# Performance work log

Hardware: AMD Instinct MI355X
Metric: run time of the kernel (lower is better)

## Reference

```python
import jax, jax.numpy as jnp
import numpy as np

N_NODES = 100000

def gcn_conv(x, edge_index, W, b):
    # torch_geometric GCNConv: add self-loops, sym-normalize, aggregate, add bias
    n = x.shape[0]
    loop = jnp.arange(n)
    src = jnp.concatenate([edge_index[0], loop])  # [E+N]
    dst = jnp.concatenate([edge_index[1], loop])
    h = x @ W  # [N, out]
    deg = jax.ops.segment_sum(jnp.ones_like(dst, dtype=h.dtype), dst, num_segments=n)
    dinv = jnp.where(deg > 0, jax.lax.rsqrt(deg), 0.0)
    norm = dinv[src] * dinv[dst]  # [E+N]
    msg = h[src] * norm[:, None]  # gather + scale
    out = jax.ops.segment_sum(msg, dst, num_segments=n)  # scatter-add
    return out + b

def setup_inputs() -> dict:
    key = jax.random.key(0)
    ks = jax.random.split(key, 6)
    N, F, H, C, E = N_NODES, 128, 128, 32, 1600000
    x = jax.random.normal(ks[0], (N, F), dtype=jnp.float32)
    edge_index = jax.random.randint(ks[1], (2, E), 0, N, dtype=jnp.int64)
    W1 = jax.random.normal(ks[2], (F, H), dtype=jnp.float32) * (1.0 / np.sqrt(F))
    b1 = jnp.zeros((H,), jnp.float32)
    W2 = jax.random.normal(ks[3], (H, H), dtype=jnp.float32) * (1.0 / np.sqrt(H))
    b2 = jnp.zeros((H,), jnp.float32)
    Wc = jax.random.normal(ks[4], (H, C), dtype=jnp.float32) * (1.0 / np.sqrt(H))
    bc = jnp.zeros((C,), jnp.float32)
    return {"x": x, "edge_index": edge_index, "W1": W1, "b1": b1, "W2": W2, "b2": b2, "Wc": Wc, "bc": bc}

def reference(x, edge_index, W1, b1, W2, b2, Wc, bc):
    h = jax.nn.relu(gcn_conv(x, edge_index, W1, b1))
    # dropout is identity in eval mode
    h = jax.nn.relu(gcn_conv(h, edge_index, W2, b2))
    pooled = jnp.mean(h, axis=0)  # [H]
    return pooled @ Wc + bc  # [C]
```

## Files before the change

### kernel.cpp

```cpp
#include <hip/hip_runtime.h>
#include <hip/hip_bf16.h>


#define FEAT 128
#define CHUNK 4096
#define MAXBUCK 512
#define ECAP 12288
#define PBLK 512
#define BPAD 16384

typedef __attribute__((ext_vector_type(8))) short short8;
typedef __attribute__((ext_vector_type(4))) float float4v;
typedef __attribute__((ext_vector_type(2))) float floatx2;

union I4S8 { int4 i; short8 s; };

static __device__ inline unsigned short f2bf(float f) {
    union { __hip_bfloat16 h; unsigned short u; } cv;
    cv.h = __float2bfloat16(f);
    return cv.u;
}

static __device__ inline floatx2 fp8x2_dec(unsigned int u) {
#if __has_builtin(__builtin_amdgcn_cvt_pk_f32_fp8)
    return __builtin_amdgcn_cvt_pk_f32_fp8((int)u, false);
#else
    floatx2 r;
    unsigned int b0 = u & 0xFFu, b1 = (u >> 8) & 0xFFu;
    r.x = __uint_as_float(((b0 & 0x80u) << 24) | ((b0 & 0x7Fu) << 20)) * 0x1p+120f;
    r.y = __uint_as_float(((b1 & 0x80u) << 24) | ((b1 & 0x7Fu) << 20)) * 0x1p+120f;
    return r;
#endif
}

static __device__ inline floatx2 fp8x2_dec_hi(unsigned int u) {
#if __has_builtin(__builtin_amdgcn_cvt_pk_f32_fp8)
    return __builtin_amdgcn_cvt_pk_f32_fp8((int)u, true);
#else
    return fp8x2_dec(u >> 16);
#endif
}

static __device__ inline unsigned short fp8x2_enc(float x, float y) {
#if __has_builtin(__builtin_amdgcn_cvt_pk_fp8_f32)
    return (unsigned short)(__builtin_amdgcn_cvt_pk_fp8_f32(x, y, 0, false) & 0xFFFF);
#else
    auto enc1 = [](float f) -> unsigned int {
        unsigned int u = __float_as_uint(f);
        unsigned int s = (u >> 24) & 0x80u;
        float a = fabsf(f);
        a = fminf(a, 448.0f);
        unsigned int code;
        if (a < 0.015625f) {
            code = (unsigned int)(int)rintf(a * 512.0f);
        } else {
            unsigned int au = __float_as_uint(a);
            unsigned int r = au + 0x0007FFFFu + ((au >> 20) & 1u);
            unsigned int e = (r >> 23) - 120u;
            unsigned int m = (r >> 20) & 7u;
            code = (e << 3) | m;
            if (code > 0x7Eu) code = 0x7Eu;
        }
        return code | s;
    };
    return (unsigned short)(enc1(x) | (enc1(y) << 8));
#endif
}

static __device__ inline unsigned char fp8enc(float f) {
#if __has_builtin(__builtin_amdgcn_cvt_pk_fp8_f32)
    return (unsigned char)(__builtin_amdgcn_cvt_pk_fp8_f32(f, 0.0f, 0, false) & 0xFF);
#else
    return (unsigned char)(fp8x2_enc(f, 0.0f) & 0xFF);
#endif
}

__global__ __launch_bounds__(256) void hist2(const int* __restrict__ dst,
                                             int* __restrict__ hist,
                                             int nE, int NC, int nbuck) {
    __shared__ int h[MAXBUCK];
    int c = blockIdx.x, t = threadIdx.x;
    for (int i = t; i < nbuck; i += 256) h[i] = 0;
    __syncthreads();
    int beg = c * CHUNK, end = min(nE, beg + CHUNK);
    for (int e = beg + t; e < end; e += 256)
        atomicAdd(&h[dst[e] >> 8], 1);
    __syncthreads();
    for (int i = t; i < nbuck; i += 256) hist[i * NC + c] = h[i];
}

__global__ __launch_bounds__(256) void rowsum_k(const int* __restrict__ hist,
                                                int* __restrict__ btot, int NC) {
    __shared__ int red[256];
    int b = blockIdx.x, t = threadIdx.x;
    int s = 0;
    for (int c = t; c < NC; c += 256) s += hist[b * NC + c];
    red[t] = s;
    __syncthreads();
    for (int o = 128; o > 0; o >>= 1) {
        if (t < o) red[t] += red[t + o];
        __syncthreads();
    }
    if (t == 0) btot[b] = red[0];
}

__global__ __launch_bounds__(512) void bscan_k(const int* __restrict__ btot,
                                               int* __restrict__ bboff, int nbuck) {
    __shared__ int sc[512];
    int t = threadIdx.x;
    int v = (t < nbuck) ? btot[t] : 0;
    sc[t] = v;
    __syncthreads();
    for (int o = 1; o < 512; o <<= 1) {
        int add = (t >= o) ? sc[t - o] : 0;
        __syncthreads();
        sc[t] += add;
        __syncthreads();
    }
    if (t < nbuck) {
        bboff[t] = sc[t] - v;
        if (t == nbuck - 1) bboff[nbuck] = sc[t];
    }
}

__global__ __launch_bounds__(512) void rowoff_k(const int* __restrict__ hist,
                                                const int* __restrict__ bboff,
                                                int* __restrict__ hoff, int NC) {
    __shared__ int sc[512];
    int b = blockIdx.x, t = threadIdx.x;
    int v = (t < NC) ? hist[b * NC + t] : 0;
    sc[t] = v;
    __syncthreads();
    for (int o = 1; o < 512; o <<= 1) {
        int add = (t >= o) ? sc[t - o] : 0;
        __syncthreads();
        sc[t] += add;
        __syncthreads();
    }
    if (t < NC) hoff[b * NC + t] = bboff[b] + sc[t] - v;
}

__global__ __launch_bounds__(256) void fill2(const int* __restrict__ src,
                                             const int* __restrict__ dst,
                                             const int* __restrict__ off,
                                             int* __restrict__ binned,
                                             int nE, int NC, int nbuck) {
    __shared__ int cur[MAXBUCK];
    int c = blockIdx.x, t = threadIdx.x;
    for (int i = t; i < nbuck; i += 256) cur[i] = off[i * NC + c];
    __syncthreads();
    int beg = c * CHUNK, end = min(nE, beg + CHUNK);
    for (int e = beg + t; e < end; e += 256) {
        int d = dst[e];
        int pos = atomicAdd(&cur[d >> 8], 1);
        binned[pos] = (src[e] << 8) | (d & 255);
    }
}

__global__ __launch_bounds__(256) void bucket_scat(const int* __restrict__ binned,
                                                   const int* __restrict__ bboff,
                                                   int* __restrict__ cnt,
                                                   float* __restrict__ dinv,
                                                   int* __restrict__ cursor,
                                                   int* __restrict__ csr_src, int n) {
    __shared__ int se[ECAP];
    __shared__ int lcnt[256];
    __shared__ int lcur[256];
    __shared__ int ssc[256];
    __shared__ int poff[128];
    int b = blockIdx.x, t = threadIdx.x;
    int node0 = b << 8;
    int nloc = min(256, n - node0);
    int ebeg = bboff[b], eend = bboff[b + 1];
    int ne = eend - ebeg;
    int pbase = (ebeg + b * BPAD + 15) & ~15;
    int zOff = n << 7;
    lcnt[t] = 0;
    lcur[t] = 0;
    __syncthreads();
    bool staged = (ne <= ECAP);
    if (staged) {
        for (int i = t; i < ne; i += 256) {
            int e = binned[ebeg + i];
            se[i] = e;
            atomicAdd(&lcnt[e & 255], 1);
        }
    } else {
        for (int i = t; i < ne; i += 256)
            atomicAdd(&lcnt[binned[ebeg + i] & 255], 1);
    }
    __syncthreads();
    int myc = (t < nloc) ? lcnt[t] : 0;
    int npair = (nloc + 1) >> 1;
    int pairSlots = 0;
    if (t < npair) {
        int mx = max(lcnt[2 * t], lcnt[2 * t + 1]);
        pairSlots = 2 * ((mx + 15) & ~15);
    }
    ssc[t] = pairSlots;
    __syncthreads();
    for (int o = 1; o < 256; o <<= 1) {
        int add = (t >= o) ? ssc[t - o] : 0;
        __syncthreads();
        ssc[t] += add;
        __syncthreads();
    }
    if (t < npair) poff[t] = ssc[t] - pairSlots;
    __syncthreads();
    if (t < nloc) {
        int p = t >> 1;
        int pl = ((max(lcnt[p * 2], lcnt[p * 2 + 1]) + 15) & ~15);
        cnt[node0 + t] = pl;
        dinv[node0 + t] = rsqrtf((float)(myc + 1));
        cursor[node0 + t] = pbase + poff[p];
    }
    __syncthreads();
    if (staged) {
        for (int i = t; i < ne; i += 256) {
            int e = se[i];
            int loc = e & 255;
            int q = atomicAdd(&lcur[loc], 1);
            int slot = pbase + poff[loc >> 1] + ((q >> 4) << 5) + ((loc & 1) << 4) + (q & 15);
            csr_src[slot] = (int)(((unsigned int)e >> 8) << 7);
        }
    } else {
        for (int i = t; i < ne; i += 256) {
            int e = binned[ebeg + i];
            int loc = e & 255;
            int q = atomicAdd(&lcur[loc], 1);
            int slot = pbase + poff[loc >> 1] + ((q >> 4) << 5) + ((loc & 1) << 4) + (q & 15);
            csr_src[slot] = (int)(((unsigned int)e >> 8) << 7);
        }
    }
    int nlocp = (nloc + 1) & ~1;
    if (t < nlocp) {
        int p = t >> 1, h = t & 1;
        int pl = ((max(lcnt[p * 2], lcnt[p * 2 + 1]) + 15) & ~15);
        int base = pbase + poff[p] + (h << 4);
        for (int q = myc; q < pl; q++)
            csr_src[base + ((q >> 4) << 5) + (q & 15)] = zOff;
    }
}

__global__ __launch_bounds__(256) void wprep2(const float* __restrict__ W1,
                                              const float* __restrict__ W2,
                                              unsigned short* __restrict__ Wbf1,
                                              unsigned short* __restrict__ Wbf2,
                                              unsigned char* __restrict__ gbuf,
                                              int n) {
    int tid = blockIdx.x * 256 + threadIdx.x;
    if (tid < 32)
        ((unsigned int*)(gbuf + (size_t)n * FEAT))[tid] = 0u;
    const float* W = (tid < 16384) ? W1 : W2;
    unsigned short* O = (tid < 16384) ? Wbf1 : Wbf2;
    int id = tid & 16383;
    int chunk = id >> 3, j = id & 7;
    int kb = chunk >> 7, nn = chunk & 127;
    O[id] = f2bf(W[(kb * 8 + j) * FEAT + nn]);
}

template <bool AFP32>
__global__ __launch_bounds__(256) void gemm_mfma(const void* __restrict__ Xv,
                                                 const unsigned short* __restrict__ Wbf,
                                                 const float* __restrict__ dinv,
                                                 unsigned char* __restrict__ gout,
                                                 int n) {
    int wave = threadIdx.x >> 6, lane = threadIdx.x & 63;
    int m0 = blockIdx.x * 64 + wave * 16;
    if (m0 >= n) return;
    int col = lane & 15, quad = lane >> 4;
    int mc = min(m0 + col, n - 1);

    short8 afr[4];
    if (AFP32) {
        const float* X = (const float*)Xv;
        const float* xr = X + (size_t)mc * FEAT + quad * 8;
#pragma unroll
        for (int ks = 0; ks < 4; ks++) {
            float4 lo = *(const float4*)(xr + ks * 32);
            float4 hi = *(const float4*)(xr + ks * 32 + 4);
            short8 a;
            a[0] = (short)f2bf(lo.x); a[1] = (short)f2bf(lo.y);
            a[2] = (short)f2bf(lo.z); a[3] = (short)f2bf(lo.w);
            a[4] = (short)f2bf(hi.x); a[5] = (short)f2bf(hi.y);
            a[6] = (short)f2bf(hi.z); a[7] = (short)f2bf(hi.w);
            afr[ks] = a;
        }
    } else {
        const unsigned char* X8 = (const unsigned char*)Xv;
        const unsigned char* xr = X8 + (size_t)mc * FEAT + quad * 8;
#pragma unroll
        for (int ks = 0; ks < 4; ks++) {
            uint2 u2 = *(const uint2*)(xr + ks * 32);
            floatx2 p0 = fp8x2_dec(u2.x);
            floatx2 p1 = fp8x2_dec_hi(u2.x);
            floatx2 p2 = fp8x2_dec(u2.y);
            floatx2 p3 = fp8x2_dec_hi(u2.y);
            short8 a;
            a[0] = (short)f2bf(p0.x); a[1] = (short)f2bf(p0.y);
            a[2] = (short)f2bf(p1.x); a[3] = (short)f2bf(p1.y);
            a[4] = (short)f2bf(p2.x); a[5] = (short)f2bf(p2.y);
            a[6] = (short)f2bf(p3.x); a[7] = (short)f2bf(p3.y);
            afr[ks] = a;
        }
    }

    float dvr[4];
#pragma unroll
    for (int r = 0; r < 4; r++)
        dvr[r] = dinv[min(m0 + quad * 4 + r, n - 1)];

    const int4* Wb = (const int4*)Wbf;
#pragma unroll
    for (int nt = 0; nt < 8; nt++) {
        float4v acc = {0.f, 0.f, 0.f, 0.f};
#pragma unroll
        for (int ks = 0; ks < 4; ks++) {
            int kb = ks * 4 + quad;
            I4S8 u; u.i = Wb[kb * FEAT + nt * 16 + col];
            acc = __builtin_amdgcn_mfma_f32_16x16x32_bf16(afr[ks], u.s, acc, 0, 0, 0);
        }
#pragma unroll
        for (int r = 0; r < 4; r++) {
            int row = m0 + quad * 4 + r;
            if (row < n)
                gout[(size_t)row * FEAT + nt * 16 + col] = fp8enc(acc[r] * dvr[r]);
        }
    }
}

__global__ __launch_bounds__(256) void agg_csr(const int* __restrict__ cursor,
                                               const int* __restrict__ cnt,
                                               const int* __restrict__ csr_src,
                                               const unsigned char* __restrict__ gbuf,
                                               const float* __restrict__ dinv,
                                               const float* __restrict__ bias,
                                               unsigned char* __restrict__ outb,
                                               int n) {
    int pair = blockIdx.x * 4 + (threadIdx.x >> 6);
    int nodeA = pair << 1;
    if (nodeA >= n) return;
    unsigned lane = threadIdx.x & 63;
    unsigned half = lane >> 5;
    unsigned sub = lane & 31;
    int node = nodeA + (int)half;
    unsigned fb = sub << 2;

    int curS = __builtin_amdgcn_readfirstlane(cursor[nodeA]);
    int plS = __builtin_amdgcn_readfirstlane(cnt[nodeA]);
    const unsigned char* csrB = (const unsigned char*)csr_src;
    const unsigned char* ip0 = csrB + (((size_t)(unsigned)curS) << 2) + (half << 6);

    unsigned su = *(const unsigned*)(gbuf + ((((unsigned)node) << 7) | fb));
    floatx2 a01 = fp8x2_dec(su), a23 = fp8x2_dec_hi(su);
    floatx2 b01 = {0.f, 0.f}, b23 = {0.f, 0.f};

    int rounds = plS >> 4;
    for (int r = 0; r < rounds; r++) {
        const unsigned char* p = ip0 + ((size_t)(unsigned)r << 7);
        int4 w0 = *(const int4*)(p);
        int4 w1 = *(const int4*)(p + 16);
        int4 w2 = *(const int4*)(p + 32);
        int4 w3 = *(const int4*)(p + 48);
        unsigned uu[16];
        uu[0]  = *(const unsigned*)(gbuf + ((unsigned)w0.x | fb));
        uu[1]  = *(const unsigned*)(gbuf + ((unsigned)w0.y | fb));
        uu[2]  = *(const unsigned*)(gbuf + ((unsigned)w0.z | fb));
        uu[3]  = *(const unsigned*)(gbuf + ((unsigned)w0.w | fb));
        uu[4]  = *(const unsigned*)(gbuf + ((unsigned)w1.x | fb));
        uu[5]  = *(const unsigned*)(gbuf + ((unsigned)w1.y | fb));
        uu[6]  = *(const unsigned*)(gbuf + ((unsigned)w1.z | fb));
        uu[7]  = *(const unsigned*)(gbuf + ((unsigned)w1.w | fb));
        uu[8]  = *(const unsigned*)(gbuf + ((unsigned)w2.x | fb));
        uu[9]  = *(const unsigned*)(gbuf + ((unsigned)w2.y | fb));
        uu[10] = *(const unsigned*)(gbuf + ((unsigned)w2.z | fb));
        uu[11] = *(const unsigned*)(gbuf + ((unsigned)w2.w | fb));
        uu[12] = *(const unsigned*)(gbuf + ((unsigned)w3.x | fb));
        uu[13] = *(const unsigned*)(gbuf + ((unsigned)w3.y | fb));
        uu[14] = *(const unsigned*)(gbuf + ((unsigned)w3.z | fb));
        uu[15] = *(const unsigned*)(gbuf + ((unsigned)w3.w | fb));
#pragma unroll
        for (int k = 0; k < 16; k += 2) {
            a01 += fp8x2_dec(uu[k]);
            a23 += fp8x2_dec_hi(uu[k]);
            b01 += fp8x2_dec(uu[k + 1]);
            b23 += fp8x2_dec_hi(uu[k + 1]);
        }
    }
    a01 += b01;
    a23 += b23;
    float dv = dinv[node];
    float4 bv = ((const float4*)bias)[sub];
    float r0 = fmaxf(a01.x * dv + bv.x, 0.0f);
    float r1 = fmaxf(a01.y * dv + bv.y, 0.0f);
    float r2 = fmaxf(a23.x * dv + bv.z, 0.0f);
    float r3 = fmaxf(a23.y * dv + bv.w, 0.0f);
    unsigned outw = (unsigned)fp8x2_enc(r0, r1) | ((unsigned)fp8x2_enc(r2, r3) << 16);
    *(unsigned*)(outb + ((((unsigned)node) << 7) | fb)) = outw;
}

__global__ __launch_bounds__(256) void pool_kernel(const unsigned char* __restrict__ a,
                                                   float* __restrict__ partial, int n) {
    __shared__ float red[16][132];
    int t = threadIdx.x, b = blockIdx.x;
    int fg = t & 15;
    int rg = t >> 4;
    unsigned fb = (unsigned)fg << 3;
    floatx2 s01 = {0.f, 0.f}, s23 = {0.f, 0.f}, s45 = {0.f, 0.f}, s67 = {0.f, 0.f};
    for (int i = (b << 4) | rg; i < n; i += PBLK * 16) {
        uint2 u2 = *(const uint2*)(a + (((unsigned)i << 7) | fb));
        s01 += fp8x2_dec(u2.x);
        s23 += fp8x2_dec_hi(u2.x);
        s45 += fp8x2_dec(u2.y);
        s67 += fp8x2_dec_hi(u2.y);
    }
    red[rg][fb + 0] = s01.x; red[rg][fb + 1] = s01.y;
    red[rg][fb + 2] = s23.x; red[rg][fb + 3] = s23.y;
    red[rg][fb + 4] = s45.x; red[rg][fb + 5] = s45.y;
    red[rg][fb + 6] = s67.x; red[rg][fb + 7] = s67.y;
    __syncthreads();
    if (t < FEAT) {
        float s = 0.0f;
#pragma unroll
        for (int k = 0; k < 16; k++) s += red[k][t];
        partial[b * FEAT + t] = s;
    }
}

__global__ __launch_bounds__(128) void final_kernel(const float* __restrict__ partial,
                                                    const float* __restrict__ Wc,
                                                    const float* __restrict__ bc,
                                                    float* __restrict__ out,
                                                    int n, int C) {
    __shared__ float p[FEAT];
    int t = threadIdx.x;
    float s = 0.0f;
    for (int b = 0; b < PBLK; b++) s += partial[b * FEAT + t];
    p[t] = s * (1.0f / (float)n);
    __syncthreads();
    if (t < C) {
        float acc = bc[t];
        for (int h = 0; h < FEAT; h++)
            acc += p[h] * Wc[h * C + t];
        out[t] = acc;
    }
}

extern "C" void kernel_launch(void* const* d_in, const int* in_sizes, int n_in,
                              void* d_out, int out_size, void* d_ws, size_t ws_size,
                              hipStream_t stream) {
    const float* x  = (const float*)d_in[0];
    const int*   ei = (const int*)d_in[1];
    const float* W1 = (const float*)d_in[2];
    const float* b1 = (const float*)d_in[3];
    const float* W2 = (const float*)d_in[4];
    const float* b2 = (const float*)d_in[5];
    const float* Wc = (const float*)d_in[6];
    const float* bc = (const float*)d_in[7];

    const int N = in_sizes[0] / FEAT;
    const int E = in_sizes[1] / 2;
    const int C = out_size;
    const int* srcI = ei;
    const int* dstI = ei + E;
    const int NC = (E + CHUNK - 1) / CHUNK;
    const int NBK = (N + 255) >> 8;
    const size_t csrCap = (size_t)E + (size_t)NBK * BPAD + 64;

    auto align256 = [](size_t v) { return (v + 255) & ~(size_t)255; };
    char* w = (char*)d_ws;
    int*            cnt     = (int*)w;            w += align256((size_t)N * 4);
    float*          dinv    = (float*)w;          w += align256((size_t)N * 4);
    int*            cursor  = (int*)w;            w += align256((size_t)N * 4);
    int*            csr_src = (int*)w;            w += align256(csrCap * 4);
    int*            binned  = (int*)w;            w += align256((size_t)E * 4);
    int*            hist    = (int*)w;            w += align256((size_t)NBK * NC * 4);
    int*            hoff    = (int*)w;            w += align256((size_t)NBK * NC * 4);
    int*            btot    = (int*)w;            w += align256((size_t)NBK * 4);
    int*            bboff   = (int*)w;            w += align256((size_t)(NBK + 1) * 4);
    unsigned short* Wbf1    = (unsigned short*)w; w += align256((size_t)FEAT * FEAT * 2);
    unsigned short* Wbf2    = (unsigned short*)w; w += align256((size_t)FEAT * FEAT * 2);
    unsigned char*  gbuf    = (unsigned char*)w;  w += align256((size_t)(N + 1) * FEAT);
    unsigned char*  bufA    = (unsigned char*)w;  w += align256((size_t)N * FEAT);
    float*          partial = (float*)w;          w += align256((size_t)PBLK * FEAT * 4);

    wprep2<<<128, 256, 0, stream>>>(W1, W2, Wbf1, Wbf2, gbuf, N);

    hist2<<<NC, 256, 0, stream>>>(dstI, hist, E, NC, NBK);
    rowsum_k<<<NBK, 256, 0, stream>>>(hist, btot, NC);
    bscan_k<<<1, 512, 0, stream>>>(btot, bboff, NBK);
    rowoff_k<<<NBK, 512, 0, stream>>>(hist, bboff, hoff, NC);
    fill2<<<NC, 256, 0, stream>>>(srcI, dstI, hoff, binned, E, NC, NBK);
    bucket_scat<<<NBK, 256, 0, stream>>>(binned, bboff, cnt, dinv, cursor, csr_src, N);

    const int gGemm = (N + 63) / 64;
    const int gAgg = (N + 7) / 8;

    gemm_mfma<true><<<gGemm, 256, 0, stream>>>(x, Wbf1, dinv, gbuf, N);
    agg_csr<<<gAgg, 256, 0, stream>>>(cursor, cnt, csr_src, gbuf, dinv, b1,
                                      bufA, N);

    gemm_mfma<false><<<gGemm, 256, 0, stream>>>(bufA, Wbf2, dinv, gbuf, N);
    agg_csr<<<gAgg, 256, 0, stream>>>(cursor, cnt, csr_src, gbuf, dinv, b2,
                                      bufA, N);

    pool_kernel<<<PBLK, 256, 0, stream>>>(bufA, partial, N);
    final_kernel<<<1, 128, 0, stream>>>(partial, Wc, bc, (float*)d_out, N, C);
}
```

Measured before the change: 266.6 us.

## Aggregate four nodes per wavefront with quad-interleaved padded CSR layout

The padded CSR layout now groups destination nodes in quads instead of pairs, interleaving 16-edge rounds for four nodes. Each wavefront aggregates four nodes, with 16 lanes per node each loading 8 fp8 features (uint2) instead of 4. This halves the number of wavefronts and makes each gather wider, but padding grows to the maximum degree among four nodes, adding dummy gathers, and the CSR buffer capacity is enlarged to match.

After: 283.2 us. 1.06x slower.

```diff
diff --git a/kernel.cpp b/kernel.cpp
--- a/kernel.cpp
+++ b/kernel.cpp
@@ -7,7 +7,7 @@
 #define MAXBUCK 512
 #define ECAP 12288
 #define PBLK 512
-#define BPAD 16384
+#define BPADQ 3904
 
 typedef __attribute__((ext_vector_type(8))) short short8;
 typedef __attribute__((ext_vector_type(4))) float float4v;
@@ -167,13 +167,13 @@
     __shared__ int lcnt[256];
     __shared__ int lcur[256];
     __shared__ int ssc[256];
-    __shared__ int poff[128];
+    __shared__ int qoff[64];
     int b = blockIdx.x, t = threadIdx.x;
     int node0 = b << 8;
     int nloc = min(256, n - node0);
     int ebeg = bboff[b], eend = bboff[b + 1];
     int ne = eend - ebeg;
-    int pbase = (ebeg + b * BPAD + 15) & ~15;
+    int pbase = (4 * ebeg + b * BPADQ + 15) & ~15;
     int zOff = n << 7;
     lcnt[t] = 0;
     lcur[t] = 0;
@@ -191,13 +191,14 @@
     }
     __syncthreads();
     int myc = (t < nloc) ? lcnt[t] : 0;
-    int npair = (nloc + 1) >> 1;
-    int pairSlots = 0;
-    if (t < npair) {
-        int mx = max(lcnt[2 * t], lcnt[2 * t + 1]);
-        pairSlots = 2 * ((mx + 15) & ~15);
-    }
-    ssc[t] = pairSlots;
+    int nquad = (nloc + 3) >> 2;
+    int quadSlots = 0;
+    if (t < nquad) {
+        int mx = max(max(lcnt[4 * t], lcnt[4 * t + 1]),
+                     max(lcnt[4 * t + 2], lcnt[4 * t + 3]));
+        quadSlots = ((mx + 15) & ~15) << 2;
+    }
+    ssc[t] = quadSlots;
     __syncthreads();
     for (int o = 1; o < 256; o <<= 1) {
         int add = (t >= o) ? ssc[t - o] : 0;
@@ -205,14 +206,15 @@
         ssc[t] += add;
         __syncthreads();
     }
-    if (t < npair) poff[t] = ssc[t] - pairSlots;
+    if (t < nquad) qoff[t] = ssc[t] - quadSlots;
     __syncthreads();
     if (t < nloc) {
-        int p = t >> 1;
-        int pl = ((max(lcnt[p * 2], lcnt[p * 2 + 1]) + 15) & ~15);
-        cnt[node0 + t] = pl;
+        int q = t >> 2;
+        int mx = max(max(lcnt[4 * q], lcnt[4 * q + 1]),
+                     max(lcnt[4 * q + 2], lcnt[4 * q + 3]));
+        cnt[node0 + t] = (mx + 15) & ~15;
         dinv[node0 + t] = rsqrtf((float)(myc + 1));
-        cursor[node0 + t] = pbase + poff[p];
+        cursor[node0 + t] = pbase + qoff[q];
     }
     __syncthreads();
     if (staged) {
@@ -220,7 +222,7 @@
             int e = se[i];
             int loc = e & 255;
             int q = atomicAdd(&lcur[loc], 1);
-            int slot = pbase + poff[loc >> 1] + ((q >> 4) << 5) + ((loc & 1) << 4) + (q & 15);
+            int slot = pbase + qoff[loc >> 2] + ((q >> 4) << 6) + ((loc & 3) << 4) + (q & 15);
             csr_src[slot] = (int)(((unsigned int)e >> 8) << 7);
         }
     } else {
@@ -228,17 +230,20 @@
             int e = binned[ebeg + i];
             int loc = e & 255;
             int q = atomicAdd(&lcur[loc], 1);
-            int slot = pbase + poff[loc >> 1] + ((q >> 4) << 5) + ((loc & 1) << 4) + (q & 15);
+            int slot = pbase + qoff[loc >> 2] + ((q >> 4) << 6) + ((loc & 3) << 4) + (q & 15);
             csr_src[slot] = (int)(((unsigned int)e >> 8) << 7);
         }
     }
-    int nlocp = (nloc + 1) & ~1;
-    if (t < nlocp) {
-        int p = t >> 1, h = t & 1;
-        int pl = ((max(lcnt[p * 2], lcnt[p * 2 + 1]) + 15) & ~15);
-        int base = pbase + poff[p] + (h << 4);
-        for (int q = myc; q < pl; q++)
-            csr_src[base + ((q >> 4) << 5) + (q & 15)] = zOff;
+    int nlocq = nquad << 2;
+    if (t < nlocq) {
+        int q = t >> 2, h = t & 3;
+        int mx = max(max(lcnt[4 * q], lcnt[4 * q + 1]),
+                     max(lcnt[4 * q + 2], lcnt[4 * q + 3]));
+        int ql = (mx + 15) & ~15;
+        int myc2 = (t < nloc) ? lcnt[t] : 0;
+        int base = pbase + qoff[q] + (h << 4);
+        for (int qp = myc2; qp < ql; qp++)
+            csr_src[base + ((qp >> 4) << 6) + (qp & 15)] = zOff;
     }
 }
 
@@ -337,66 +342,75 @@
                                                const float* __restrict__ bias,
                                                unsigned char* __restrict__ outb,
                                                int n) {
-    int pair = blockIdx.x * 4 + (threadIdx.x >> 6);
-    int nodeA = pair << 1;
+    int quad = blockIdx.x * 4 + (threadIdx.x >> 6);
+    int nodeA = quad << 2;
     if (nodeA >= n) return;
     unsigned lane = threadIdx.x & 63;
-    unsigned half = lane >> 5;
-    unsigned sub = lane & 31;
-    int node = nodeA + (int)half;
-    unsigned fb = sub << 2;
+    unsigned h = lane >> 4;
+    unsigned sub = lane & 15;
+    int node = nodeA + (int)h;
+    bool act = node < n;
+    int nodeC = act ? node : (n - 1);
+    unsigned fb = sub << 3;
 
     int curS = __builtin_amdgcn_readfirstlane(cursor[nodeA]);
-    int plS = __builtin_amdgcn_readfirstlane(cnt[nodeA]);
+    int qlS  = __builtin_amdgcn_readfirstlane(cnt[nodeA]);
     const unsigned char* csrB = (const unsigned char*)csr_src;
-    const unsigned char* ip0 = csrB + (((size_t)(unsigned)curS) << 2) + (half << 6);
-
-    unsigned su = *(const unsigned*)(gbuf + ((((unsigned)node) << 7) | fb));
-    floatx2 a01 = fp8x2_dec(su), a23 = fp8x2_dec_hi(su);
-    floatx2 b01 = {0.f, 0.f}, b23 = {0.f, 0.f};
-
-    int rounds = plS >> 4;
+    const unsigned char* ip0 = csrB + (((size_t)(unsigned)curS) << 2) + (h << 6);
+
+    uint2 su = *(const uint2*)(gbuf + ((((unsigned)nodeC) << 7) | fb));
+    floatx2 a01 = fp8x2_dec(su.x), a23 = fp8x2_dec_hi(su.x);
+    floatx2 a45 = fp8x2_dec(su.y), a67 = fp8x2_dec_hi(su.y);
+
+    int rounds = qlS >> 4;
     for (int r = 0; r < rounds; r++) {
-        const unsigned char* p = ip0 + ((size_t)(unsigned)r << 7);
+        const unsigned char* p = ip0 + ((size_t)(unsigned)r << 8);
         int4 w0 = *(const int4*)(p);
         int4 w1 = *(const int4*)(p + 16);
         int4 w2 = *(const int4*)(p + 32);
         int4 w3 = *(const int4*)(p + 48);
-        unsigned uu[16];
-        uu[0]  = *(const unsigned*)(gbuf + ((unsigned)w0.x | fb));
-        uu[1]  = *(const unsigned*)(gbuf + ((unsigned)w0.y | fb));
-        uu[2]  = *(const unsigned*)(gbuf + ((unsigned)w0.z | fb));
-        uu[3]  = *(const unsigned*)(gbuf + ((unsigned)w0.w | fb));
-        uu[4]  = *(const unsigned*)(gbuf + ((unsigned)w1.x | fb));
-        uu[5]  = *(const unsigned*)(gbuf + ((unsigned)w1.y | fb));
-        uu[6]  = *(const unsigned*)(gbuf + ((unsigned)w1.z | fb));
-        uu[7]  = *(const unsigned*)(gbuf + ((unsigned)w1.w | fb));
-        uu[8]  = *(const unsigned*)(gbuf + ((unsigned)w2.x | fb));
-        uu[9]  = *(const unsigned*)(gbuf + ((unsigned)w2.y | fb));
-        uu[10] = *(const unsigned*)(gbuf + ((unsigned)w2.z | fb));
-        uu[11] = *(const unsigned*)(gbuf + ((unsigned)w2.w | fb));
-        uu[12] = *(const unsigned*)(gbuf + ((unsigned)w3.x | fb));
-        uu[13] = *(const unsigned*)(gbuf + ((unsigned)w3.y | fb));
-        uu[14] = *(const unsigned*)(gbuf + ((unsigned)w3.z | fb));
-        uu[15] = *(const unsigned*)(gbuf + ((unsigned)w3.w | fb));
-#pragma unroll
-        for (int k = 0; k < 16; k += 2) {
-            a01 += fp8x2_dec(uu[k]);
-            a23 += fp8x2_dec_hi(uu[k]);
-            b01 += fp8x2_dec(uu[k + 1]);
-            b23 += fp8x2_dec_hi(uu[k + 1]);
-        }
-    }
-    a01 += b01;
-    a23 += b23;
-    float dv = dinv[node];
-    float4 bv = ((const float4*)bias)[sub];
-    float r0 = fmaxf(a01.x * dv + bv.x, 0.0f);
-    float r1 = fmaxf(a01.y * dv + bv.y, 0.0f);
-    float r2 = fmaxf(a23.x * dv + bv.z, 0.0f);
-    float r3 = fmaxf(a23.y * dv + bv.w, 0.0f);
-    unsigned outw = (unsigned)fp8x2_enc(r0, r1) | ((unsigned)fp8x2_enc(r2, r3) << 16);
-    *(unsigned*)(outb + ((((unsigned)node) << 7) | fb)) = outw;
+        uint2 uu[16];
+        uu[0]  = *(const uint2*)(gbuf + ((unsigned)w0.x | fb));
+        uu[1]  = *(const uint2*)(gbuf + ((unsigned)w0.y | fb));
+        uu[2]  = *(const uint2*)(gbuf + ((unsigned)w0.z | fb));
+        uu[3]  = *(const uint2*)(gbuf + ((unsigned)w0.w | fb));
+        uu[4]  = *(const uint2*)(gbuf + ((unsigned)w1.x | fb));
+        uu[5]  = *(const uint2*)(gbuf + ((unsigned)w1.y | fb));
+        uu[6]  = *(const uint2*)(gbuf + ((unsigned)w1.z | fb));
+        uu[7]  = *(const uint2*)(gbuf + ((unsigned)w1.w | fb));
+        uu[8]  = *(const uint2*)(gbuf + ((unsigned)w2.x | fb));
+        uu[9]  = *(const uint2*)(gbuf + ((unsigned)w2.y | fb));
+        uu[10] = *(const uint2*)(gbuf + ((unsigned)w2.z | fb));
+        uu[11] = *(const uint2*)(gbuf + ((unsigned)w2.w | fb));
+        uu[12] = *(const uint2*)(gbuf + ((unsigned)w3.x | fb));
+        uu[13] = *(const uint2*)(gbuf + ((unsigned)w3.y | fb));
+        uu[14] = *(const uint2*)(gbuf + ((unsigned)w3.z | fb));
+        uu[15] = *(const uint2*)(gbuf + ((unsigned)w3.w | fb));
+#pragma unroll
+        for (int k = 0; k < 16; k++) {
+            a01 += fp8x2_dec(uu[k].x);
+            a23 += fp8x2_dec_hi(uu[k].x);
+            a45 += fp8x2_dec(uu[k].y);
+            a67 += fp8x2_dec_hi(uu[k].y);
+        }
+    }
+    if (act) {
+        float dv = dinv[node];
+        const float4* b4 = (const float4*)bias;
+        float4 bv0 = b4[sub * 2], bv1 = b4[sub * 2 + 1];
+        float r0 = fmaxf(a01.x * dv + bv0.x, 0.0f);
+        float r1 = fmaxf(a01.y * dv + bv0.y, 0.0f);
+        float r2 = fmaxf(a23.x * dv + bv0.z, 0.0f);
+        float r3 = fmaxf(a23.y * dv + bv0.w, 0.0f);
+        float r4 = fmaxf(a45.x * dv + bv1.x, 0.0f);
+        float r5 = fmaxf(a45.y * dv + bv1.y, 0.0f);
+        float r6 = fmaxf(a67.x * dv + bv1.z, 0.0f);
+        float r7 = fmaxf(a67.y * dv + bv1.w, 0.0f);
+        uint2 ow;
+        ow.x = (unsigned)fp8x2_enc(r0, r1) | ((unsigned)fp8x2_enc(r2, r3) << 16);
+        ow.y = (unsigned)fp8x2_enc(r4, r5) | ((unsigned)fp8x2_enc(r6, r7) << 16);
+        *(uint2*)(outb + ((((unsigned)node) << 7) | fb)) = ow;
+    }
 }
 
 __global__ __launch_bounds__(256) void pool_kernel(const unsigned char* __restrict__ a,
@@ -465,7 +479,7 @@
     const int* dstI = ei + E;
     const int NC = (E + CHUNK - 1) / CHUNK;
     const int NBK = (N + 255) >> 8;
-    const size_t csrCap = (size_t)E + (size_t)NBK * BPAD + 64;
+    const size_t csrCap = (size_t)4 * E + (size_t)NBK * BPADQ + 64;
 
     auto align256 = [](size_t v) { return (v + 255) & ~(size_t)255; };
     char* w = (char*)d_ws;
@@ -494,7 +508,7 @@
     bucket_scat<<<NBK, 256, 0, stream>>>(binned, bboff, cnt, dinv, cursor, csr_src, N);
 
     const int gGemm = (N + 63) / 64;
-    const int gAgg = (N + 7) / 8;
+    const int gAgg = (N + 15) / 16;
 
     gemm_mfma<true><<<gGemm, 256, 0, stream>>>(x, Wbf1, dinv, gbuf, N);
     agg_csr<<<gAgg, 256, 0, stream>>>(cursor, cnt, csr_src, gbuf, dinv, b1,
```

## Replace bucketed two-pass CSR build with per-node global atomic histogram and scatter

Applied to the files above, without the earlier changes.

Replaces the chunked bucket histogram, row offsets, binning and per-bucket shared-memory scatter with a simpler pipeline. It counts in-degrees with global atomics per node, computes padded pair slots and bucket offsets from those counts, pads slots, then scatters edges directly with per-node global atomic cursors. This drops two kernels and the intermediate binned array, trading them for random global atomics and scattered writes into the CSR buffer.

Result: slower. 412.2 us (+54.6%).

```diff
diff --git a/kernel.cpp b/kernel.cpp
--- a/kernel.cpp
+++ b/kernel.cpp
@@ -3,11 +3,7 @@
 
 
 #define FEAT 128
-#define CHUNK 4096
-#define MAXBUCK 512
-#define ECAP 12288
 #define PBLK 512
-#define BPAD 16384
 
 typedef __attribute__((ext_vector_type(8))) short short8;
 typedef __attribute__((ext_vector_type(4))) float float4v;
@@ -75,33 +71,36 @@
 #endif
 }
 
-__global__ __launch_bounds__(256) void hist2(const int* __restrict__ dst,
-                                             int* __restrict__ hist,
-                                             int nE, int NC, int nbuck) {
-    __shared__ int h[MAXBUCK];
-    int c = blockIdx.x, t = threadIdx.x;
-    for (int i = t; i < nbuck; i += 256) h[i] = 0;
-    __syncthreads();
-    int beg = c * CHUNK, end = min(nE, beg + CHUNK);
-    for (int e = beg + t; e < end; e += 256)
-        atomicAdd(&h[dst[e] >> 8], 1);
-    __syncthreads();
-    for (int i = t; i < nbuck; i += 256) hist[i * NC + c] = h[i];
-}
-
-__global__ __launch_bounds__(256) void rowsum_k(const int* __restrict__ hist,
-                                                int* __restrict__ btot, int NC) {
-    __shared__ int red[256];
+__global__ __launch_bounds__(256) void histN(const int* __restrict__ dst,
+                                             int* __restrict__ cnt, int nE) {
+    int stride = gridDim.x * 256;
+    for (int e = blockIdx.x * 256 + threadIdx.x; e < nE; e += stride)
+        atomicAdd(&cnt[dst[e]], 1);
+}
+
+__global__ __launch_bounds__(256) void pairsum_k(const int* __restrict__ cnt,
+                                                 int* __restrict__ btot, int n) {
+    __shared__ int lcnt[256];
+    __shared__ int ssc[256];
     int b = blockIdx.x, t = threadIdx.x;
-    int s = 0;
-    for (int c = t; c < NC; c += 256) s += hist[b * NC + c];
-    red[t] = s;
-    __syncthreads();
-    for (int o = 128; o > 0; o >>= 1) {
-        if (t < o) red[t] += red[t + o];
-        __syncthreads();
-    }
-    if (t == 0) btot[b] = red[0];
+    int node0 = b << 8;
+    int nloc = min(256, n - node0);
+    lcnt[t] = (t < nloc) ? cnt[node0 + t] : 0;
+    __syncthreads();
+    int pairSlots = 0;
+    if (t < 128) {
+        int mx = max(lcnt[2 * t], lcnt[2 * t + 1]);
+        pairSlots = ((mx + 15) & ~15) << 1;
+    }
+    ssc[t] = pairSlots;
+    __syncthreads();
+    for (int o = 1; o < 256; o <<= 1) {
+        int add = (t >= o) ? ssc[t - o] : 0;
+        __syncthreads();
+        ssc[t] += add;
+        __syncthreads();
+    }
+    if (t == 255) btot[b] = ssc[255];
 }
 
 __global__ __launch_bounds__(512) void bscan_k(const int* __restrict__ btot,
@@ -123,79 +122,26 @@
     }
 }
 
-__global__ __launch_bounds__(512) void rowoff_k(const int* __restrict__ hist,
-                                                const int* __restrict__ bboff,
-                                                int* __restrict__ hoff, int NC) {
-    __shared__ int sc[512];
-    int b = blockIdx.x, t = threadIdx.x;
-    int v = (t < NC) ? hist[b * NC + t] : 0;
-    sc[t] = v;
-    __syncthreads();
-    for (int o = 1; o < 512; o <<= 1) {
-        int add = (t >= o) ? sc[t - o] : 0;
-        __syncthreads();
-        sc[t] += add;
-        __syncthreads();
-    }
-    if (t < NC) hoff[b * NC + t] = bboff[b] + sc[t] - v;
-}
-
-__global__ __launch_bounds__(256) void fill2(const int* __restrict__ src,
-                                             const int* __restrict__ dst,
-                                             const int* __restrict__ off,
-                                             int* __restrict__ binned,
-                                             int nE, int NC, int nbuck) {
-    __shared__ int cur[MAXBUCK];
-    int c = blockIdx.x, t = threadIdx.x;
-    for (int i = t; i < nbuck; i += 256) cur[i] = off[i * NC + c];
-    __syncthreads();
-    int beg = c * CHUNK, end = min(nE, beg + CHUNK);
-    for (int e = beg + t; e < end; e += 256) {
-        int d = dst[e];
-        int pos = atomicAdd(&cur[d >> 8], 1);
-        binned[pos] = (src[e] << 8) | (d & 255);
-    }
-}
-
-__global__ __launch_bounds__(256) void bucket_scat(const int* __restrict__ binned,
+__global__ __launch_bounds__(256) void cursorpad_k(int* __restrict__ cnt,
                                                    const int* __restrict__ bboff,
-                                                   int* __restrict__ cnt,
+                                                   int* __restrict__ cursor,
                                                    float* __restrict__ dinv,
-                                                   int* __restrict__ cursor,
+                                                   int* __restrict__ qcur,
                                                    int* __restrict__ csr_src, int n) {
-    __shared__ int se[ECAP];
     __shared__ int lcnt[256];
-    __shared__ int lcur[256];
     __shared__ int ssc[256];
     __shared__ int poff[128];
     int b = blockIdx.x, t = threadIdx.x;
     int node0 = b << 8;
     int nloc = min(256, n - node0);
-    int ebeg = bboff[b], eend = bboff[b + 1];
-    int ne = eend - ebeg;
-    int pbase = (ebeg + b * BPAD + 15) & ~15;
+    int pbase = bboff[b];
     int zOff = n << 7;
-    lcnt[t] = 0;
-    lcur[t] = 0;
-    __syncthreads();
-    bool staged = (ne <= ECAP);
-    if (staged) {
-        for (int i = t; i < ne; i += 256) {
-            int e = binned[ebeg + i];
-            se[i] = e;
-            atomicAdd(&lcnt[e & 255], 1);
-        }
-    } else {
-        for (int i = t; i < ne; i += 256)
-            atomicAdd(&lcnt[binned[ebeg + i] & 255], 1);
-    }
-    __syncthreads();
-    int myc = (t < nloc) ? lcnt[t] : 0;
-    int npair = (nloc + 1) >> 1;
+    lcnt[t] = (t < nloc) ? cnt[node0 + t] : 0;
+    __syncthreads();
     int pairSlots = 0;
-    if (t < npair) {
+    if (t < 128) {
         int mx = max(lcnt[2 * t], lcnt[2 * t + 1]);
-        pairSlots = 2 * ((mx + 15) & ~15);
+        pairSlots = ((mx + 15) & ~15) << 1;
     }
     ssc[t] = pairSlots;
     __syncthreads();
@@ -205,40 +151,38 @@
         ssc[t] += add;
         __syncthreads();
     }
-    if (t < npair) poff[t] = ssc[t] - pairSlots;
-    __syncthreads();
+    if (t < 128) poff[t] = ssc[t] - pairSlots;
+    __syncthreads();
+    int p = t >> 1, h = t & 1;
+    int pl = ((max(lcnt[p * 2], lcnt[p * 2 + 1]) + 15) & ~15);
     if (t < nloc) {
-        int p = t >> 1;
-        int pl = ((max(lcnt[p * 2], lcnt[p * 2 + 1]) + 15) & ~15);
+        int deg = lcnt[t];
         cnt[node0 + t] = pl;
-        dinv[node0 + t] = rsqrtf((float)(myc + 1));
+        dinv[node0 + t] = rsqrtf((float)(deg + 1));
         cursor[node0 + t] = pbase + poff[p];
-    }
-    __syncthreads();
-    if (staged) {
-        for (int i = t; i < ne; i += 256) {
-            int e = se[i];
-            int loc = e & 255;
-            int q = atomicAdd(&lcur[loc], 1);
-            int slot = pbase + poff[loc >> 1] + ((q >> 4) << 5) + ((loc & 1) << 4) + (q & 15);
-            csr_src[slot] = (int)(((unsigned int)e >> 8) << 7);
-        }
-    } else {
-        for (int i = t; i < ne; i += 256) {
-            int e = binned[ebeg + i];
-            int loc = e & 255;
-            int q = atomicAdd(&lcur[loc], 1);
-            int slot = pbase + poff[loc >> 1] + ((q >> 4) << 5) + ((loc & 1) << 4) + (q & 15);
-            csr_src[slot] = (int)(((unsigned int)e >> 8) << 7);
-        }
+        qcur[node0 + t] = 0;
     }
     int nlocp = (nloc + 1) & ~1;
     if (t < nlocp) {
-        int p = t >> 1, h = t & 1;
-        int pl = ((max(lcnt[p * 2], lcnt[p * 2 + 1]) + 15) & ~15);
+        int deg = (t < nloc) ? lcnt[t] : 0;
         int base = pbase + poff[p] + (h << 4);
-        for (int q = myc; q < pl; q++)
+        for (int q = deg; q < pl; q++)
             csr_src[base + ((q >> 4) << 5) + (q & 15)] = zOff;
+    }
+}
+
+__global__ __launch_bounds__(256) void scatter_k(const int* __restrict__ src,
+                                                 const int* __restrict__ dst,
+                                                 const int* __restrict__ cursor,
+                                                 int* __restrict__ qcur,
+                                                 int* __restrict__ csr_src, int nE) {
+    int stride = gridDim.x * 256;
+    for (int e = blockIdx.x * 256 + threadIdx.x; e < nE; e += stride) {
+        int d = dst[e];
+        int s = src[e];
+        int q = atomicAdd(&qcur[d], 1);
+        int slot = cursor[d] + ((q >> 4) << 5) + ((d & 1) << 4) + (q & 15);
+        csr_src[slot] = s << 7;
     }
 }
 
@@ -247,10 +191,12 @@
                                               unsigned short* __restrict__ Wbf1,
                                               unsigned short* __restrict__ Wbf2,
                                               unsigned char* __restrict__ gbuf,
+                                              int* __restrict__ cnt,
                                               int n) {
     int tid = blockIdx.x * 256 + threadIdx.x;
     if (tid < 32)
         ((unsigned int*)(gbuf + (size_t)n * FEAT))[tid] = 0u;
+    for (int i = tid; i < n; i += 32768) cnt[i] = 0;
     const float* W = (tid < 16384) ? W1 : W2;
     unsigned short* O = (tid < 16384) ? Wbf1 : Wbf2;
     int id = tid & 16383;
@@ -463,19 +409,16 @@
     const int C = out_size;
     const int* srcI = ei;
     const int* dstI = ei + E;
-    const int NC = (E + CHUNK - 1) / CHUNK;
     const int NBK = (N + 255) >> 8;
-    const size_t csrCap = (size_t)E + (size_t)NBK * BPAD + 64;
+    const size_t csrCap = (size_t)2 * E + (size_t)NBK * 3840 + 64;
 
     auto align256 = [](size_t v) { return (v + 255) & ~(size_t)255; };
     char* w = (char*)d_ws;
     int*            cnt     = (int*)w;            w += align256((size_t)N * 4);
     float*          dinv    = (float*)w;          w += align256((size_t)N * 4);
     int*            cursor  = (int*)w;            w += align256((size_t)N * 4);
+    int*            qcur    = (int*)w;            w += align256((size_t)N * 4);
     int*            csr_src = (int*)w;            w += align256(csrCap * 4);
-    int*            binned  = (int*)w;            w += align256((size_t)E * 4);
-    int*            hist    = (int*)w;            w += align256((size_t)NBK * NC * 4);
-    int*            hoff    = (int*)w;            w += align256((size_t)NBK * NC * 4);
     int*            btot    = (int*)w;            w += align256((size_t)NBK * 4);
     int*            bboff   = (int*)w;            w += align256((size_t)(NBK + 1) * 4);
     unsigned short* Wbf1    = (unsigned short*)w; w += align256((size_t)FEAT * FEAT * 2);
@@ -484,14 +427,13 @@
     unsigned char*  bufA    = (unsigned char*)w;  w += align256((size_t)N * FEAT);
     float*          partial = (float*)w;          w += align256((size_t)PBLK * FEAT * 4);
 
-    wprep2<<<128, 256, 0, stream>>>(W1, W2, Wbf1, Wbf2, gbuf, N);
-
-    hist2<<<NC, 256, 0, stream>>>(dstI, hist, E, NC, NBK);
-    rowsum_k<<<NBK, 256, 0, stream>>>(hist, btot, NC);
+    wprep2<<<128, 256, 0, stream>>>(W1, W2, Wbf1, Wbf2, gbuf, cnt, N);
+
+    histN<<<1563, 256, 0, stream>>>(dstI, cnt, E);
+    pairsum_k<<<NBK, 256, 0, stream>>>(cnt, btot, N);
     bscan_k<<<1, 512, 0, stream>>>(btot, bboff, NBK);
-    rowoff_k<<<NBK, 512, 0, stream>>>(hist, bboff, hoff, NC);
-    fill2<<<NC, 256, 0, stream>>>(srcI, dstI, hoff, binned, E, NC, NBK);
-    bucket_scat<<<NBK, 256, 0, stream>>>(binned, bboff, cnt, dinv, cursor, csr_src, N);
+    cursorpad_k<<<NBK, 256, 0, stream>>>(cnt, bboff, cursor, dinv, qcur, csr_src, N);
+    scatter_k<<<1563, 256, 0, stream>>>(srcI, dstI, cursor, qcur, csr_src, E);
 
     const int gGemm = (N + 63) / 64;
     const int gAgg = (N + 7) / 8;
```
